# Optimization experiments

Hardware: AMD Instinct MI355X
Metric: run time of the kernel (lower is better)

Reference implementation:

```python
import jax, jax.numpy as jnp
import numpy as np

B, S, D, H = 2, 2048, 1024, 16
HD = D // H


def setup_inputs() -> dict:
    key = jax.random.key(0)
    ks = jax.random.split(key, 12)
    sc = 0.02
    inp = {
        "q": jax.random.normal(ks[0], (B, S, D), jnp.float32),
        "k": jax.random.normal(ks[1], (B, S, D), jnp.float32),
        "v": jax.random.normal(ks[2], (B, S, D), jnp.float32),
        # causal mask, broadcastable to [B,H,S,S]; 0 => masked
        "mask": jnp.tril(jnp.ones((S, S), jnp.int32))[None, None],
        "Wq": jax.random.normal(ks[3], (D, D), jnp.float32) * sc,
        "bq": jnp.zeros((D,), jnp.float32),
        "Wk": jax.random.normal(ks[4], (D, D), jnp.float32) * sc,
        "bk": jnp.zeros((D,), jnp.float32),
        "Wv": jax.random.normal(ks[5], (D, D), jnp.float32) * sc,
        "bv": jnp.zeros((D,), jnp.float32),
        "Wf": jax.random.normal(ks[6], (D, D), jnp.float32) * sc,
        "bf": jnp.zeros((D,), jnp.float32),
    }
    return inp


def reference(q, k, v, mask, Wq, bq, Wk, bk, Wv, bv, Wf, bf):
    b = q.shape[0]
    # projections (torch Linear: x @ W.T + b)
    qh = (q @ Wq.T + bq).reshape(b, -1, H, HD).transpose(0, 2, 1, 3)  # [B,H,S,HD]
    kh = (k @ Wk.T + bk).reshape(b, -1, H, HD).transpose(0, 2, 1, 3)
    vh = (v @ Wv.T + bv).reshape(b, -1, H, HD).transpose(0, 2, 1, 3)
    scores = jnp.einsum("bhqd,bhkd->bhqk", qh, kh) / jnp.sqrt(jnp.float32(HD))
    scores = jnp.where(mask == 0, jnp.float32(-1e9), scores)
    attn = jax.nn.softmax(scores, axis=-1)
    x = jnp.einsum("bhqk,bhkd->bhqd", attn, vh)  # [B,H,S,HD]
    x = x.transpose(0, 2, 1, 3).reshape(b, -1, D)
    return x @ Wf.T + bf
```

## Files before the change

kernel.cpp:

```cpp
#include <hip/hip_runtime.h>

typedef __attribute__((ext_vector_type(4))) float f32x4;
typedef __attribute__((ext_vector_type(8))) short bf16x8;
typedef unsigned short u16;
typedef unsigned int u32;

#define QSCALE 0.18033688011112042f

__device__ __forceinline__ u16 f2bf(float f) {
  union { float f; u32 u; } v; v.f = f;
  u32 r = v.u + 0x7fffu + ((v.u >> 16) & 1u);
  return (u16)(r >> 16);
}

__device__ __forceinline__ u32 cvtpk(float a, float b) {
  u32 r;
  asm("v_cvt_pk_bf16_f32 %0, %1, %2" : "=v"(r) : "v"(a), "v"(b));
  return r;
}

__device__ __forceinline__ void gl_lds16(const u16* g, u16* l) {
  __builtin_amdgcn_global_load_lds((const __attribute__((address_space(1))) u32*)g,
                                   (__attribute__((address_space(3))) u32*)l, 16, 0, 0);
}

__global__ __launch_bounds__(256) void conv_kernel(
    const float* __restrict__ q, const float* __restrict__ k, const float* __restrict__ v,
    const float* __restrict__ wq, const float* __restrict__ wk, const float* __restrict__ wv,
    const float* __restrict__ wf, u16* __restrict__ dst)
{
  size_t i = ((size_t)blockIdx.x * 256 + threadIdx.x) * 8;
  const float* src; size_t off;
  if (i < ((size_t)3 << 22)) {
    int a = (int)(i >> 22);
    src = (a == 0) ? q : ((a == 1) ? k : v);
    off = i & ((1u << 22) - 1);
  } else {
    size_t j = i - ((size_t)3 << 22);
    int a = (int)(j >> 20);
    src = (a == 0) ? wq : ((a == 1) ? wk : ((a == 2) ? wv : wf));
    off = j & ((1u << 20) - 1);
  }
  float4 x0 = *reinterpret_cast<const float4*>(src + off);
  float4 x1 = *reinterpret_cast<const float4*>(src + off + 4);
  u32 o[4] = {cvtpk(x0.x, x0.y), cvtpk(x0.z, x0.w), cvtpk(x1.x, x1.y), cvtpk(x1.z, x1.w)};
  *reinterpret_cast<uint4*>(dst + i) = *reinterpret_cast<const uint4*>(o);
}

struct GArg {
  const u16* X; const u16* W; const float* bias; void* out; int mode; float scale;
};

template<int BM>
__global__ __launch_bounds__(256) void gemm_bf(GArg a0, GArg a1, GArg a2) {
  constexpr int K = 1024, N = 1024;
  constexpr int WNw = (BM == 128) ? 2 : 4;
  constexpr int NI  = (128 / WNw) / 16;
  constexpr int CA  = BM / 32;
  __shared__ __align__(16) u16 lA[BM * 64];
  __shared__ __align__(16) u16 lB[128 * 64];
  GArg a = (blockIdx.z == 0) ? a0 : ((blockIdx.z == 1) ? a1 : a2);
  const int m0 = blockIdx.x * BM, n0 = blockIdx.y * 128;
  const int tid = threadIdx.x, w = tid >> 6, lane = tid & 63;
  const int lr = lane & 15, lg = lane >> 4;
  const int wm = (w / WNw) * 64, wn = (w % WNw) * (128 / WNw);
  const int lrow8 = lane >> 3, lc = lane & 7;
  const int schunk = (lc ^ lrow8) * 8;

  f32x4 acc[4][NI] = {};

  for (int kt = 0; kt < K; kt += 64) {
    #pragma unroll
    for (int c = 0; c < CA; ++c) {
      int row = w * (BM / 4) + c * 8 + lrow8;
      gl_lds16(a.X + (size_t)(m0 + row) * K + kt + schunk, &lA[(w * (BM / 4) + c * 8) * 64]);
    }
    #pragma unroll
    for (int c = 0; c < 4; ++c) {
      int row = w * 32 + c * 8 + lrow8;
      gl_lds16(a.W + (size_t)(n0 + row) * K + kt + schunk, &lB[(w * 32 + c * 8) * 64]);
    }
    __syncthreads();
    #pragma unroll
    for (int h = 0; h < 2; ++h) {
      bf16x8 af[4], bfv[NI];
      #pragma unroll
      for (int i = 0; i < 4; ++i) {
        int r = wm + i * 16 + lr;
        af[i] = *reinterpret_cast<const bf16x8*>(&lA[r * 64 + (((h * 4 + lg) ^ (r & 7)) * 8)]);
      }
      #pragma unroll
      for (int i = 0; i < NI; ++i) {
        int r = wn + i * 16 + lr;
        bfv[i] = *reinterpret_cast<const bf16x8*>(&lB[r * 64 + (((h * 4 + lg) ^ (r & 7)) * 8)]);
      }
      __builtin_amdgcn_s_setprio(1);
      #pragma unroll
      for (int mi = 0; mi < 4; ++mi)
        #pragma unroll
        for (int ni = 0; ni < NI; ++ni)
          acc[mi][ni] = __builtin_amdgcn_mfma_f32_16x16x32_bf16(af[mi], bfv[ni], acc[mi][ni], 0, 0, 0);
      __builtin_amdgcn_s_setprio(0);
    }
    __syncthreads();
  }

  #pragma unroll
  for (int mi = 0; mi < 4; ++mi) {
    #pragma unroll
    for (int ni = 0; ni < NI; ++ni) {
      int col = n0 + wn + ni * 16 + lr;
      float bv = a.bias[col];
      #pragma unroll
      for (int r = 0; r < 4; ++r) {
        int row = m0 + wm + mi * 16 + lg * 4 + r;
        float val = (acc[mi][ni][r] + bv) * a.scale;
        if (a.mode == 2) {
          ((float*)a.out)[(size_t)row * N + col] = val;
        } else {
          int b = row >> 11, s = row & 2047, hh = col >> 6, hd = col & 63;
          u16* O = (u16*)a.out;
          if (a.mode == 0) O[((size_t)(b * 16 + hh) * 2048 + s) * 64 + hd] = f2bf(val);
          else             O[((size_t)(b * 16 + hh) * 64 + hd) * 2048 + s] = f2bf(val);
        }
      }
    }
  }
}

template<int IN_BF16, int OUT_MODE>
__global__ __launch_bounds__(256) void gemm_legacy(
    const void* __restrict__ Xv, const float* __restrict__ W,
    const float* __restrict__ bias, void* __restrict__ Outv, float scale)
{
  constexpr int N = 1024, K = 1024;
  __shared__ __align__(16) u16 lA[128 * 32];
  __shared__ __align__(16) u16 lB[128 * 32];
  const int n0 = blockIdx.x * 128, m0 = blockIdx.y * 128;
  const int tid = threadIdx.x;
  const int w = tid >> 6, lane = tid & 63, lr = lane & 15, lg = lane >> 4;
  const int wm = (w >> 1) * 64, wn = (w & 1) * 64;
  f32x4 acc[4][4] = {};
  for (int kt = 0; kt < K; kt += 32) {
    #pragma unroll
    for (int it = 0; it < 4; ++it) {
      int idx = it * 256 + tid, row = idx >> 3, c4 = idx & 7;
      float4 xv = *reinterpret_cast<const float4*>(&W[(size_t)(n0 + row) * K + kt + c4 * 4]);
      u16* dst = &lB[row * 32 + c4 * 4];
      dst[0] = f2bf(xv.x); dst[1] = f2bf(xv.y); dst[2] = f2bf(xv.z); dst[3] = f2bf(xv.w);
    }
    if (IN_BF16 == 0) {
      const float* X = (const float*)Xv;
      #pragma unroll
      for (int it = 0; it < 4; ++it) {
        int idx = it * 256 + tid, row = idx >> 3, c4 = idx & 7;
        float4 xv = *reinterpret_cast<const float4*>(&X[(size_t)(m0 + row) * K + kt + c4 * 4]);
        u16* dst = &lA[row * 32 + c4 * 4];
        dst[0] = f2bf(xv.x); dst[1] = f2bf(xv.y); dst[2] = f2bf(xv.z); dst[3] = f2bf(xv.w);
      }
    } else {
      const u16* X = (const u16*)Xv;
      #pragma unroll
      for (int it = 0; it < 2; ++it) {
        int idx = it * 256 + tid, row = idx >> 2, c = idx & 3;
        *reinterpret_cast<uint4*>(&lA[row * 32 + c * 8]) =
            *reinterpret_cast<const uint4*>(&X[(size_t)(m0 + row) * K + kt + c * 8]);
      }
    }
    __syncthreads();
    bf16x8 af[4], bfr[4];
    #pragma unroll
    for (int i = 0; i < 4; ++i) {
      af[i]  = *reinterpret_cast<const bf16x8*>(&lA[(wm + i * 16 + lr) * 32 + lg * 8]);
      bfr[i] = *reinterpret_cast<const bf16x8*>(&lB[(wn + i * 16 + lr) * 32 + lg * 8]);
    }
    #pragma unroll
    for (int mi = 0; mi < 4; ++mi)
      #pragma unroll
      for (int ni = 0; ni < 4; ++ni)
        acc[mi][ni] = __builtin_amdgcn_mfma_f32_16x16x32_bf16(af[mi], bfr[ni], acc[mi][ni], 0, 0, 0);
    __syncthreads();
  }
  #pragma unroll
  for (int mi = 0; mi < 4; ++mi)
    #pragma unroll
    for (int ni = 0; ni < 4; ++ni) {
      int col = n0 + wn + ni * 16 + lr;
      float bv = bias[col];
      #pragma unroll
      for (int r = 0; r < 4; ++r) {
        int row = m0 + wm + mi * 16 + lg * 4 + r;
        float val = (acc[mi][ni][r] + bv) * scale;
        if (OUT_MODE == 2) {
          ((float*)Outv)[(size_t)row * N + col] = val;
        } else {
          int b = row >> 11, s = row & 2047, h = col >> 6, hd = col & 63;
          u16* O = (u16*)Outv;
          if (OUT_MODE == 0) O[((size_t)(b * 16 + h) * 2048 + s) * 64 + hd] = f2bf(val);
          else               O[((size_t)(b * 16 + h) * 64 + hd) * 2048 + s] = f2bf(val);
        }
      }
    }
}


__device__ __forceinline__ void seg_step4(
    const bf16x8* aq, f32x4* oacc, float& ls,
    const u16* lK, const u16* lV, char* pwb,
    bool diag, int col0, int qv, int lr, int lg, bf16x8 ones)
{
  const int cs = lr & 7;
  f32x4 sc[4];
  #pragma unroll
  for (int nf = 0; nf < 4; ++nf) {
    const u16* kr = &lK[(nf * 16 + lr) * 64];
    bf16x8 k0 = *reinterpret_cast<const bf16x8*>(&kr[(lg ^ cs) * 8]);
    bf16x8 k1 = *reinterpret_cast<const bf16x8*>(&kr[((4 + lg) ^ cs) * 8]);
    f32x4 z = {};
    __builtin_amdgcn_s_setprio(1);
    z = __builtin_amdgcn_mfma_f32_16x16x32_bf16(k0, aq[0], z, 0, 0, 0);
    z = __builtin_amdgcn_mfma_f32_16x16x32_bf16(k1, aq[1], z, 0, 0, 0);
    __builtin_amdgcn_s_setprio(0);
    sc[nf] = z;
  }
  if (diag) {
    #pragma unroll
    for (int nf = 0; nf < 4; ++nf)
      #pragma unroll
      for (int r = 0; r < 4; ++r)
        if ((col0 + nf * 16 + lg * 4 + r) > qv) sc[nf][r] = -1e30f;
  }
  #pragma unroll
  for (int nf = 0; nf < 4; ++nf) {
    float p0 = exp2f(sc[nf][0]), p1 = exp2f(sc[nf][1]);
    float p2 = exp2f(sc[nf][2]), p3 = exp2f(sc[nf][3]);
    uint2 pr;
    pr.x = cvtpk(p0, p1);
    pr.y = cvtpk(p2, p3);
    *reinterpret_cast<uint2*>(pwb + lr * 128 + ((32 * nf + 8 * lg) ^ (cs << 4))) = pr;
  }
  bf16x8 pb0 = *reinterpret_cast<const bf16x8*>(pwb + lr * 128 + 16 * (lg ^ cs));
  bf16x8 pb1 = *reinterpret_cast<const bf16x8*>(pwb + lr * 128 + 16 * ((4 + lg) ^ cs));
  f32x4 rs = {};
  rs = __builtin_amdgcn_mfma_f32_16x16x32_bf16(ones, pb0, rs, 0, 0, 0);
  rs = __builtin_amdgcn_mfma_f32_16x16x32_bf16(ones, pb1, rs, 0, 0, 0);
  ls += rs[0];
  #pragma unroll
  for (int df = 0; df < 4; ++df) {
    const u16* vr = &lV[(df * 16 + lr) * 64];
    bf16x8 v0 = *reinterpret_cast<const bf16x8*>(&vr[(lg ^ cs) * 8]);
    bf16x8 v1 = *reinterpret_cast<const bf16x8*>(&vr[((4 + lg) ^ cs) * 8]);
    __builtin_amdgcn_s_setprio(1);
    oacc[df] = __builtin_amdgcn_mfma_f32_16x16x32_bf16(v0, pb0, oacc[df], 0, 0, 0);
    oacc[df] = __builtin_amdgcn_mfma_f32_16x16x32_bf16(v1, pb1, oacc[df], 0, 0, 0);
    __builtin_amdgcn_s_setprio(0);
  }
}

__global__ __launch_bounds__(256) void attn_kernel8(
    const u16* __restrict__ Qh, const u16* __restrict__ Kh,
    const u16* __restrict__ Vt, u16* __restrict__ Oa)
{
  __shared__ __align__(16) u16 lK[2][64 * 64];
  __shared__ __align__(16) u16 lV[2][64 * 64];
  __shared__ __align__(16) u16 lP[4][16 * 64];
  const int bh = blockIdx.x;
  const int t = 31 - blockIdx.y;
  const int b = bh >> 4, h = bh & 15;
  const u16* Qb = Qh + (size_t)bh * 2048 * 64;
  const u16* Kb = Kh + (size_t)bh * 2048 * 64;
  const u16* Vb = Vt + (size_t)bh * 64 * 2048;
  const int tid = threadIdx.x, w = tid >> 6, lane = tid & 63;
  const int lr = lane & 15, lg = lane >> 4;
  const int lrow8 = lane >> 3, lc = lane & 7;
  const int schunk = (lc ^ lrow8) * 8;
  char* pwb = (char*)lP[w];

  bf16x8 ones;
  #pragma unroll
  for (int j = 0; j < 8; ++j) ones[j] = (short)0x3F80;

  bf16x8 aq[2];
  {
    int qrow = t * 64 + w * 16 + lr;
    aq[0] = *reinterpret_cast<const bf16x8*>(&Qb[(size_t)qrow * 64 + lg * 8]);
    aq[1] = *reinterpret_cast<const bf16x8*>(&Qb[(size_t)qrow * 64 + 32 + lg * 8]);
  }
  f32x4 oacc[4] = {};
  float ls = 0.f;
  const int qv = t * 64 + w * 16 + lr;

  const int nkt = t + 1;
  int cur = 0;

  #pragma unroll
  for (int c = 0; c < 2; ++c) {
    int row = w * 16 + c * 8 + lrow8;
    gl_lds16(Kb + (size_t)row * 64 + schunk, &lK[0][(w * 16 + c * 8) * 64]);
    gl_lds16(Vb + (size_t)row * 2048 + schunk, &lV[0][(w * 16 + c * 8) * 64]);
  }
  __syncthreads();

  for (int kt = 0; kt < nkt; ++kt) {
    if (kt + 1 < nkt) {
      #pragma unroll
      for (int c = 0; c < 2; ++c) {
        int row = w * 16 + c * 8 + lrow8;
        gl_lds16(Kb + (size_t)((kt + 1) * 64 + row) * 64 + schunk, &lK[cur ^ 1][(w * 16 + c * 8) * 64]);
        gl_lds16(Vb + (size_t)row * 2048 + (kt + 1) * 64 + schunk, &lV[cur ^ 1][(w * 16 + c * 8) * 64]);
      }
    }
    seg_step4(aq, oacc, ls, lK[cur], lV[cur], pwb, kt == t, kt * 64, qv, lr, lg, ones);
    if (kt + 1 < nkt) __syncthreads();
    cur ^= 1;
  }

  float inv = 1.0f / ls;
  #pragma unroll
  for (int df = 0; df < 4; ++df) {
    uint2 pa;
    pa.x = cvtpk(oacc[df][0] * inv, oacc[df][1] * inv);
    pa.y = cvtpk(oacc[df][2] * inv, oacc[df][3] * inv);
    *reinterpret_cast<uint2*>(&Oa[(size_t)(b * 2048 + qv) * 1024 + h * 64 + df * 16 + lg * 4]) = pa;
  }
}

extern "C" void kernel_launch(void* const* d_in, const int* in_sizes, int n_in,
                              void* d_out, int out_size, void* d_ws, size_t ws_size,
                              hipStream_t stream) {
  const float* q  = (const float*)d_in[0];
  const float* k  = (const float*)d_in[1];
  const float* v  = (const float*)d_in[2];
  const float* Wq = (const float*)d_in[4];
  const float* bq = (const float*)d_in[5];
  const float* Wk = (const float*)d_in[6];
  const float* bk = (const float*)d_in[7];
  const float* Wv = (const float*)d_in[8];
  const float* bv = (const float*)d_in[9];
  const float* Wf = (const float*)d_in[10];
  const float* bf = (const float*)d_in[11];

  if (ws_size >= ((size_t)64 << 20)) {
    u16* wsb = (u16*)d_ws;
    u16* qb  = wsb;
    u16* kb  = wsb + (1u << 22);
    u16* vb  = wsb + ((size_t)2 << 22);
    u16* wqb = wsb + ((size_t)3 << 22);
    u16* wkb = wqb + (1u << 20);
    u16* wvb = wkb + (1u << 20);
    u16* wfb = wvb + (1u << 20);
    u16* Qh  = wsb + ((size_t)1 << 24);
    u16* Kh  = Qh + (1u << 22);
    u16* Vt  = Kh + (1u << 22);
    u16* Oa  = Vt + (1u << 22);

    conv_kernel<<<8192, 256, 0, stream>>>(q, k, v, Wq, Wk, Wv, Wf, wsb);

    GArg gq{qb, wqb, bq, Qh, 0, QSCALE};
    GArg gk{kb, wkb, bk, Kh, 0, 1.0f};
    GArg gv{vb, wvb, bv, Vt, 1, 1.0f};
    gemm_bf<128><<<dim3(32, 8, 3), 256, 0, stream>>>(gq, gk, gv);

    attn_kernel8<<<dim3(32, 32), 256, 0, stream>>>(Qh, Kh, Vt, Oa);

    GArg gf{Oa, wfb, bf, d_out, 2, 1.0f};
    gemm_bf<64><<<dim3(64, 8, 1), 256, 0, stream>>>(gf, gf, gf);
  } else {
    u16* Qh = (u16*)d_ws;
    u16* Kh = Qh + (size_t)4096 * 1024;
    u16* Vt = Kh + (size_t)4096 * 1024;
    u16* Oa = Vt + (size_t)4096 * 1024;
    dim3 gg(8, 32), gb(256);
    gemm_legacy<0, 0><<<gg, gb, 0, stream>>>(q, Wq, bq, Qh, QSCALE);
    gemm_legacy<0, 0><<<gg, gb, 0, stream>>>(k, Wk, bk, Kh, 1.0f);
    gemm_legacy<0, 1><<<gg, gb, 0, stream>>>(v, Wv, bv, Vt, 1.0f);
    attn_kernel8<<<dim3(32, 32), gb, 0, stream>>>(Qh, Kh, Vt, Oa);
    gemm_legacy<1, 2><<<gg, gb, 0, stream>>>(Oa, Wf, bf, (float*)d_out, 1.0f);
  }
}
```

Measured before the change: 112.3 us.

## Split causal attention KV range in two halves with a separate combine kernel

Each query tile's key range is split into two halves handled by separate blocks, doubling the attention grid. Each block writes an unnormalized partial output and its row sums. A new combine kernel adds the two partials, normalizes them, and writes the head-interleaved output. The aim is better load balance and occupancy across the uneven causal workload, at the cost of an extra launch and extra global traffic for the partial results. The fallback path reuses workspace buffers in a way that may overflow.

```diff
diff --git a/kernel.cpp b/kernel.cpp
--- a/kernel.cpp
+++ b/kernel.cpp
@@ -11,6 +11,10 @@
   union { float f; u32 u; } v; v.f = f;
   u32 r = v.u + 0x7fffu + ((v.u >> 16) & 1u);
   return (u16)(r >> 16);
+}
+
+__device__ __forceinline__ float bf2f(u16 x) {
+  union { u32 u; float f; } v; v.u = ((u32)x) << 16; return v.f;
 }
 
 __device__ __forceinline__ u32 cvtpk(float a, float b) {
@@ -257,16 +261,19 @@
   }
 }
 
-__global__ __launch_bounds__(256) void attn_kernel8(
+__global__ __launch_bounds__(256) void attn_kernel10(
     const u16* __restrict__ Qh, const u16* __restrict__ Kh,
-    const u16* __restrict__ Vt, u16* __restrict__ Oa)
+    const u16* __restrict__ Vt, u16* __restrict__ Op, float* __restrict__ Lp)
 {
   __shared__ __align__(16) u16 lK[2][64 * 64];
   __shared__ __align__(16) u16 lV[2][64 * 64];
   __shared__ __align__(16) u16 lP[4][16 * 64];
   const int bh = blockIdx.x;
-  const int t = 31 - blockIdx.y;
-  const int b = bh >> 4, h = bh & 15;
+  const int slot = blockIdx.y;
+  const int t = 31 - (slot >> 1);
+  const int half = slot & 1;
+  const int nk = t + 1, kh = (nk + 1) >> 1;
+  const int ks = half ? kh : 0, ke = half ? nk : kh;
   const u16* Qb = Qh + (size_t)bh * 2048 * 64;
   const u16* Kb = Kh + (size_t)bh * 2048 * 64;
   const u16* Vb = Vt + (size_t)bh * 64 * 2048;
@@ -280,49 +287,74 @@
   #pragma unroll
   for (int j = 0; j < 8; ++j) ones[j] = (short)0x3F80;
 
-  bf16x8 aq[2];
-  {
-    int qrow = t * 64 + w * 16 + lr;
-    aq[0] = *reinterpret_cast<const bf16x8*>(&Qb[(size_t)qrow * 64 + lg * 8]);
-    aq[1] = *reinterpret_cast<const bf16x8*>(&Qb[(size_t)qrow * 64 + 32 + lg * 8]);
-  }
   f32x4 oacc[4] = {};
   float ls = 0.f;
   const int qv = t * 64 + w * 16 + lr;
 
-  const int nkt = t + 1;
-  int cur = 0;
-
-  #pragma unroll
-  for (int c = 0; c < 2; ++c) {
-    int row = w * 16 + c * 8 + lrow8;
-    gl_lds16(Kb + (size_t)row * 64 + schunk, &lK[0][(w * 16 + c * 8) * 64]);
-    gl_lds16(Vb + (size_t)row * 2048 + schunk, &lV[0][(w * 16 + c * 8) * 64]);
-  }
-  __syncthreads();
-
-  for (int kt = 0; kt < nkt; ++kt) {
-    if (kt + 1 < nkt) {
-      #pragma unroll
-      for (int c = 0; c < 2; ++c) {
-        int row = w * 16 + c * 8 + lrow8;
-        gl_lds16(Kb + (size_t)((kt + 1) * 64 + row) * 64 + schunk, &lK[cur ^ 1][(w * 16 + c * 8) * 64]);
-        gl_lds16(Vb + (size_t)row * 2048 + (kt + 1) * 64 + schunk, &lV[cur ^ 1][(w * 16 + c * 8) * 64]);
-      }
-    }
-    seg_step4(aq, oacc, ls, lK[cur], lV[cur], pwb, kt == t, kt * 64, qv, lr, lg, ones);
-    if (kt + 1 < nkt) __syncthreads();
-    cur ^= 1;
-  }
-
-  float inv = 1.0f / ls;
+  if (ks < ke) {
+    bf16x8 aq[2];
+    {
+      int qrow = t * 64 + w * 16 + lr;
+      aq[0] = *reinterpret_cast<const bf16x8*>(&Qb[(size_t)qrow * 64 + lg * 8]);
+      aq[1] = *reinterpret_cast<const bf16x8*>(&Qb[(size_t)qrow * 64 + 32 + lg * 8]);
+    }
+    int cur = 0;
+    #pragma unroll
+    for (int c = 0; c < 2; ++c) {
+      int row = w * 16 + c * 8 + lrow8;
+      gl_lds16(Kb + (size_t)(ks * 64 + row) * 64 + schunk, &lK[0][(w * 16 + c * 8) * 64]);
+      gl_lds16(Vb + (size_t)row * 2048 + ks * 64 + schunk, &lV[0][(w * 16 + c * 8) * 64]);
+    }
+    __syncthreads();
+
+    for (int kt = ks; kt < ke; ++kt) {
+      if (kt + 1 < ke) {
+        #pragma unroll
+        for (int c = 0; c < 2; ++c) {
+          int row = w * 16 + c * 8 + lrow8;
+          gl_lds16(Kb + (size_t)((kt + 1) * 64 + row) * 64 + schunk, &lK[cur ^ 1][(w * 16 + c * 8) * 64]);
+          gl_lds16(Vb + (size_t)row * 2048 + (kt + 1) * 64 + schunk, &lV[cur ^ 1][(w * 16 + c * 8) * 64]);
+        }
+      }
+      seg_step4(aq, oacc, ls, lK[cur], lV[cur], pwb, kt == t, kt * 64, qv, lr, lg, ones);
+      if (kt + 1 < ke) __syncthreads();
+      cur ^= 1;
+    }
+  }
+
+  const int p = (bh * 32 + t) * 2 + half;
+  const int qloc = w * 16 + lr;
   #pragma unroll
   for (int df = 0; df < 4; ++df) {
     uint2 pa;
-    pa.x = cvtpk(oacc[df][0] * inv, oacc[df][1] * inv);
-    pa.y = cvtpk(oacc[df][2] * inv, oacc[df][3] * inv);
-    *reinterpret_cast<uint2*>(&Oa[(size_t)(b * 2048 + qv) * 1024 + h * 64 + df * 16 + lg * 4]) = pa;
-  }
+    pa.x = cvtpk(oacc[df][0], oacc[df][1]);
+    pa.y = cvtpk(oacc[df][2], oacc[df][3]);
+    *reinterpret_cast<uint2*>(&Op[(((size_t)p * 64 + qloc) * 64) + df * 16 + lg * 4]) = pa;
+  }
+  if (lg == 0) Lp[(size_t)p * 64 + qloc] = ls;
+}
+
+__global__ __launch_bounds__(256) void combine_kernel(
+    const u16* __restrict__ Op, const float* __restrict__ Lp, u16* __restrict__ Oa)
+{
+  const int bh = blockIdx.x, t = blockIdx.y;
+  const int b = bh >> 4, h = bh & 15;
+  const int tid = threadIdx.x;
+  const int q = tid >> 2, d0 = (tid & 3) * 16;
+  const size_t p0 = ((size_t)(bh * 32 + t)) * 2, p1 = p0 + 1;
+  float inv = 1.0f / (Lp[p0 * 64 + q] + Lp[p1 * 64 + q]);
+  const u16* s0 = Op + (p0 * 64 + q) * 64 + d0;
+  const u16* s1 = Op + (p1 * 64 + q) * 64 + d0;
+  u32 o[8];
+  #pragma unroll
+  for (int i = 0; i < 8; ++i) {
+    float a0 = bf2f(s0[2 * i])     + bf2f(s1[2 * i]);
+    float a1 = bf2f(s0[2 * i + 1]) + bf2f(s1[2 * i + 1]);
+    o[i] = cvtpk(a0 * inv, a1 * inv);
+  }
+  u16* dst = Oa + ((size_t)(b * 2048 + t * 64 + q)) * 1024 + h * 64 + d0;
+  *reinterpret_cast<uint4*>(dst)     = *reinterpret_cast<const uint4*>(&o[0]);
+  *reinterpret_cast<uint4*>(dst + 8) = *reinterpret_cast<const uint4*>(&o[4]);
 }
 
 extern "C" void kernel_launch(void* const* d_in, const int* in_sizes, int n_in,
@@ -353,6 +385,8 @@
     u16* Kh  = Qh + (1u << 22);
     u16* Vt  = Kh + (1u << 22);
     u16* Oa  = Vt + (1u << 22);
+    u16*   Op = qb;
+    float* Lp = (float*)(wsb + ((size_t)2048 * 4096));
 
     conv_kernel<<<8192, 256, 0, stream>>>(q, k, v, Wq, Wk, Wv, Wf, wsb);
 
@@ -361,7 +395,8 @@
     GArg gv{vb, wvb, bv, Vt, 1, 1.0f};
     gemm_bf<128><<<dim3(32, 8, 3), 256, 0, stream>>>(gq, gk, gv);
 
-    attn_kernel8<<<dim3(32, 32), 256, 0, stream>>>(Qh, Kh, Vt, Oa);
+    attn_kernel10<<<dim3(32, 64), 256, 0, stream>>>(Qh, Kh, Vt, Op, Lp);
+    combine_kernel<<<dim3(32, 32), 256, 0, stream>>>(Op, Lp, Oa);
 
     GArg gf{Oa, wfb, bf, d_out, 2, 1.0f};
     gemm_bf<64><<<dim3(64, 8, 1), 256, 0, stream>>>(gf, gf, gf);
@@ -374,7 +409,10 @@
     gemm_legacy<0, 0><<<gg, gb, 0, stream>>>(q, Wq, bq, Qh, QSCALE);
     gemm_legacy<0, 0><<<gg, gb, 0, stream>>>(k, Wk, bk, Kh, 1.0f);
     gemm_legacy<0, 1><<<gg, gb, 0, stream>>>(v, Wv, bv, Vt, 1.0f);
-    attn_kernel8<<<dim3(32, 32), gb, 0, stream>>>(Qh, Kh, Vt, Oa);
-    gemm_legacy<1, 2><<<gg, gb, 0, stream>>>(Oa, Wf, bf, (float*)d_out, 1.0f);
-  }
-}
+    u16*   Op2 = Oa;
+    float* Lp2 = (float*)(Qh);
+    attn_kernel10<<<dim3(32, 64), gb, 0, stream>>>(Qh, Kh, Vt, Op2, (float*)(Op2 + (size_t)2048 * 4096 - 2048 * 64 * 2));
+    combine_kernel<<<dim3(32, 32), gb, 0, stream>>>(Op2, (float*)(Op2 + (size_t)2048 * 4096 - 2048 * 64 * 2), Qh);
+    gemm_legacy<1, 2><<<gg, gb, 0, stream>>>(Qh, Wf, bf, (float*)d_out, 1.0f);
+  }
+}
```

Result: slower. 115.2 us (+2.6%).

## Process 128 query rows per attention block with 8 waves sharing K/V tiles

Applied to the files above, without the earlier changes.

The attention kernel now uses 512 threads (8 waves) so each block covers 128 query rows instead of 64, and the grid shrinks to 32x16. Each K/V tile loaded into LDS is shared by twice as many waves, halving global K/V traffic per query row. Each wave loads one 8-row slice of the tile. Waves in the first half stop one tile earlier, since their diagonal comes one tile sooner, but they still wait at the barriers. This costs some idle time on the causal boundary, and there are fewer, larger blocks, which may hurt load balance and occupancy.

```diff
diff --git a/kernel.cpp b/kernel.cpp
--- a/kernel.cpp
+++ b/kernel.cpp
@@ -257,15 +257,15 @@
   }
 }
 
-__global__ __launch_bounds__(256) void attn_kernel8(
+__global__ __launch_bounds__(512) void attn_kernel11(
     const u16* __restrict__ Qh, const u16* __restrict__ Kh,
     const u16* __restrict__ Vt, u16* __restrict__ Oa)
 {
   __shared__ __align__(16) u16 lK[2][64 * 64];
   __shared__ __align__(16) u16 lV[2][64 * 64];
-  __shared__ __align__(16) u16 lP[4][16 * 64];
+  __shared__ __align__(16) u16 lP[8][16 * 64];
   const int bh = blockIdx.x;
-  const int t = 31 - blockIdx.y;
+  const int T = 15 - blockIdx.y;
   const int b = bh >> 4, h = bh & 15;
   const u16* Qb = Qh + (size_t)bh * 2048 * 64;
   const u16* Kb = Kh + (size_t)bh * 2048 * 64;
@@ -281,36 +281,31 @@
   for (int j = 0; j < 8; ++j) ones[j] = (short)0x3F80;
 
   bf16x8 aq[2];
-  {
-    int qrow = t * 64 + w * 16 + lr;
-    aq[0] = *reinterpret_cast<const bf16x8*>(&Qb[(size_t)qrow * 64 + lg * 8]);
-    aq[1] = *reinterpret_cast<const bf16x8*>(&Qb[(size_t)qrow * 64 + 32 + lg * 8]);
-  }
+  const int qrow = T * 128 + w * 16 + lr;
+  aq[0] = *reinterpret_cast<const bf16x8*>(&Qb[(size_t)qrow * 64 + lg * 8]);
+  aq[1] = *reinterpret_cast<const bf16x8*>(&Qb[(size_t)qrow * 64 + 32 + lg * 8]);
+
   f32x4 oacc[4] = {};
   float ls = 0.f;
-  const int qv = t * 64 + w * 16 + lr;
-
-  const int nkt = t + 1;
+  const int qv = qrow;
+
+  const int nkt = 2 * T + 2;
+  const int mydiag = 2 * T + (w >> 2);
+  const int myend = mydiag + 1;
+  const int srow = w * 8 + lrow8;
   int cur = 0;
 
-  #pragma unroll
-  for (int c = 0; c < 2; ++c) {
-    int row = w * 16 + c * 8 + lrow8;
-    gl_lds16(Kb + (size_t)row * 64 + schunk, &lK[0][(w * 16 + c * 8) * 64]);
-    gl_lds16(Vb + (size_t)row * 2048 + schunk, &lV[0][(w * 16 + c * 8) * 64]);
-  }
+  gl_lds16(Kb + (size_t)srow * 64 + schunk, &lK[0][(w * 8) * 64]);
+  gl_lds16(Vb + (size_t)srow * 2048 + schunk, &lV[0][(w * 8) * 64]);
   __syncthreads();
 
   for (int kt = 0; kt < nkt; ++kt) {
     if (kt + 1 < nkt) {
-      #pragma unroll
-      for (int c = 0; c < 2; ++c) {
-        int row = w * 16 + c * 8 + lrow8;
-        gl_lds16(Kb + (size_t)((kt + 1) * 64 + row) * 64 + schunk, &lK[cur ^ 1][(w * 16 + c * 8) * 64]);
-        gl_lds16(Vb + (size_t)row * 2048 + (kt + 1) * 64 + schunk, &lV[cur ^ 1][(w * 16 + c * 8) * 64]);
-      }
-    }
-    seg_step4(aq, oacc, ls, lK[cur], lV[cur], pwb, kt == t, kt * 64, qv, lr, lg, ones);
+      gl_lds16(Kb + (size_t)((kt + 1) * 64 + srow) * 64 + schunk, &lK[cur ^ 1][(w * 8) * 64]);
+      gl_lds16(Vb + (size_t)srow * 2048 + (kt + 1) * 64 + schunk, &lV[cur ^ 1][(w * 8) * 64]);
+    }
+    if (kt < myend)
+      seg_step4(aq, oacc, ls, lK[cur], lV[cur], pwb, kt == mydiag, kt * 64, qv, lr, lg, ones);
     if (kt + 1 < nkt) __syncthreads();
     cur ^= 1;
   }
@@ -361,7 +356,7 @@
     GArg gv{vb, wvb, bv, Vt, 1, 1.0f};
     gemm_bf<128><<<dim3(32, 8, 3), 256, 0, stream>>>(gq, gk, gv);
 
-    attn_kernel8<<<dim3(32, 32), 256, 0, stream>>>(Qh, Kh, Vt, Oa);
+    attn_kernel11<<<dim3(32, 16), 512, 0, stream>>>(Qh, Kh, Vt, Oa);
 
     GArg gf{Oa, wfb, bf, d_out, 2, 1.0f};
     gemm_bf<64><<<dim3(64, 8, 1), 256, 0, stream>>>(gf, gf, gf);
@@ -374,7 +369,7 @@
     gemm_legacy<0, 0><<<gg, gb, 0, stream>>>(q, Wq, bq, Qh, QSCALE);
     gemm_legacy<0, 0><<<gg, gb, 0, stream>>>(k, Wk, bk, Kh, 1.0f);
     gemm_legacy<0, 1><<<gg, gb, 0, stream>>>(v, Wv, bv, Vt, 1.0f);
-    attn_kernel8<<<dim3(32, 32), gb, 0, stream>>>(Qh, Kh, Vt, Oa);
+    attn_kernel11<<<dim3(32, 16), 512, 0, stream>>>(Qh, Kh, Vt, Oa);
     gemm_legacy<1, 2><<<gg, gb, 0, stream>>>(Oa, Wf, bf, (float*)d_out, 1.0f);
   }
 }
```

Result: slower. 118.0 us (+5.1%).
